# Performance work log

Hardware: AMD Instinct MI355X
Metric: run time of the kernel (lower is better)

Reference implementation:

```python
import jax, jax.numpy as jnp
import numpy as np

N = 262144            # inflated nodes (atoms + edge-nodes)
E = 4 * 1024 * 1024   # directed edges
D = 8                 # node_feature_dim
TD = 1                # time_dim
H = 32                # hidden_channels
L = 4                 # num_layers
BN_EPS = 1e-5


def setup_inputs() -> dict:
    key = jax.random.key(0)
    ks = jax.random.split(key, 12)
    s = 0.1  # small init scale
    return {
        "x": jax.random.normal(ks[0], (N, D), jnp.float32),
        "t": jax.random.uniform(ks[1], (1,), jnp.float32),
        "edge_index": jax.random.randint(ks[2], (2, E), 0, N, jnp.int32),
        "node_mask": jax.random.randint(ks[3], (N,), 0, 2) > 0,
        "edge_mask": jax.random.randint(ks[4], (N,), 0, 2) > 0,
        "ond": 5,  # original_node_feature_dim
        "oed": 4,  # original_edge_feature_dim
        # GINConv MLP params: layer 0 has in=D+TD, layers 1..3 have in=H
        "W1_first": jax.random.normal(ks[5], (D + TD, H), jnp.float32) * s,
        "b1_first": jnp.zeros((H,), jnp.float32),
        "W2_first": jax.random.normal(ks[6], (H, H), jnp.float32) * s,
        "b2_first": jnp.zeros((H,), jnp.float32),
        "W1_rest": jax.random.normal(ks[7], (L - 1, H, H), jnp.float32) * s,
        "b1_rest": jnp.zeros((L - 1, H), jnp.float32),
        "W2_rest": jax.random.normal(ks[8], (L - 1, H, H), jnp.float32) * s,
        "b2_rest": jnp.zeros((L - 1, H), jnp.float32),
        "eps": jnp.zeros((L,), jnp.float32),           # train_eps=True, init 0
        "bn_gamma": jnp.ones((L, H), jnp.float32),
        "bn_beta": jnp.zeros((L, H), jnp.float32),
        "lin_W": jax.random.normal(ks[9], (L * H, D), jnp.float32) * s,
        "lin_b": jnp.zeros((D,), jnp.float32),
    }


def _gin_forward(x, t, W1_first, b1_first, W2_first, b2_first,
                 W1_rest, b1_rest, W2_rest, b2_rest, eps, bn_gamma, bn_beta,
                 lin_W, lin_b, edge_index, node_mask, edge_mask, ond, oed):
    src = edge_index[0]
    dst = edge_index[1]
    n = x.shape[0]
    # x_in = cat(x, t*ones)
    tcol = jnp.full((n, 1), t[0], x.dtype)
    h = jnp.concatenate([x, tcol], axis=1)  # [N, D+TD]
    xs = []
    for l in range(L):
        # GINConv: (1+eps)*x_i + sum_{j->i} x_j, then 2-layer MLP
        agg = jax.ops.segment_sum(h[src], dst, num_segments=n)  # scatter-add
        z = (1.0 + eps[l]) * h + agg
        W1 = W1_first if l == 0 else W1_rest[l - 1]
        b1 = b1_first if l == 0 else b1_rest[l - 1]
        W2 = W2_first if l == 0 else W2_rest[l - 1]
        b2 = b2_first if l == 0 else b2_rest[l - 1]
        z = jax.nn.relu(z @ W1 + b1) @ W2 + b2  # [N, H]
        # BatchNorm (training-mode batch stats), then ReLU; dropout=eval->id
        mu = jnp.mean(z, axis=0)
        var = jnp.var(z, axis=0)
        z = (z - mu) * jax.lax.rsqrt(var + BN_EPS) * bn_gamma[l] + bn_beta[l]
        h = jax.nn.relu(z)
        xs.append(h)
    # JK 'cat' + final Linear(L*H -> D)
    new_x = jnp.concatenate(xs, axis=1) @ lin_W + lin_b  # [N, D]
    # masked feature write-back: x[mask, 1:dim+1] = new_x[mask, 1:dim+1]
    cols = jnp.arange(x.shape[1])
    ncols = (cols >= 1) & (cols < ond + 1)
    ecols = (cols >= 1) & (cols < oed + 1)
    out = jnp.where(node_mask[:, None] & ncols[None, :], new_x, x)
    out = jnp.where(edge_mask[:, None] & ecols[None, :], new_x, out)
    return out


def reference(x, t, edge_index, node_mask, edge_mask, ond, oed,
              W1_first, b1_first, W2_first, b2_first,
              W1_rest, b1_rest, W2_rest, b2_rest,
              eps, bn_gamma, bn_beta, lin_W, lin_b):
    return _gin_forward(x, t, W1_first, b1_first, W2_first, b2_first,
                        W1_rest, b1_rest, W2_rest, b2_rest,
                        eps, bn_gamma, bn_beta, lin_W, lin_b,
                        edge_index, node_mask, edge_mask, ond, oed)
```

## Files before the change

kernel.cpp:

```cpp
#include <hip/hip_runtime.h>
#include <cstdint>

#define NN 262144
#define EE 4194304
#define CAP 64
#define NB 512
#define BSZ 512
#define NSH 8
#define SCAP 1280
#define EPB 4096
#define SLICES 64

typedef __attribute__((ext_vector_type(8))) short bf16x8;
typedef __attribute__((ext_vector_type(4))) float f32x4;
typedef __attribute__((ext_vector_type(2))) float f32x2;
#define MFMA16 __builtin_amdgcn_mfma_f32_16x16x32_bf16

__device__ inline float bf2f(unsigned short u) {
  union { unsigned int i; float f; } v; v.i = ((unsigned int)u) << 16; return v.f;
}
__device__ inline unsigned short f2bf(float f) {
  union { float f; unsigned int i; } v; v.f = f;
  unsigned int r = v.i + 0x7FFF + ((v.i >> 16) & 1);
  return (unsigned short)(r >> 16);
}
__device__ inline float blo(unsigned int u) {
  union { unsigned int i; float f; } v; v.i = u << 16; return v.f;
}
__device__ inline float bhi(unsigned int u) {
  union { unsigned int i; float f; } v; v.i = u & 0xFFFF0000u; return v.f;
}
__device__ inline f32x2 bfpair(unsigned int u) {
  union { unsigned int i; float f; } lo, hi;
  lo.i = u << 16; hi.i = u & 0xFFFF0000u;
  return (f32x2){lo.f, hi.f};
}

__global__ void k_prep(int* __restrict__ cur,
                       const float* __restrict__ W1f, const float* __restrict__ W2f,
                       const float* __restrict__ W1r, const float* __restrict__ W2r,
                       unsigned short* __restrict__ wimg) {
  int tid = threadIdx.x;
  if (blockIdx.x < 16) {
    int i = blockIdx.x * 256 + tid;
    if (i < NSH * NB) cur[i] = i * SCAP;
    return;
  }
  for (int k = tid; k < 4 * 4 * 1280; k += 256) wimg[k] = 0;
  __syncthreads();
  for (int l = 0; l < 4; ++l) {
    const float* W1 = (l == 0) ? W1f : W1r + (size_t)(l - 1) * 1024;
    const float* W2 = (l == 0) ? W2f : W2r + (size_t)(l - 1) * 1024;
    int kdim = (l == 0) ? 9 : 32;
    unsigned short* bm = wimg + (size_t)l * 5120;
    for (int e = tid; e < kdim * 32; e += 256) {
      int k = e >> 5, n = e & 31;
      float v = W1[e];
      unsigned short h = f2bf(v);
      int idx = n * 40 + (k ^ (n & 8));
      bm[idx] = h;
      bm[1280 + idx] = f2bf(v - bf2f(h));
    }
    for (int e = tid; e < 1024; e += 256) {
      int k = e >> 5, n = e & 31;
      float v = W2[e];
      unsigned short h = f2bf(v);
      int idx = n * 40 + (k ^ (n & 8));
      bm[2560 + idx] = h;
      bm[3840 + idx] = f2bf(v - bf2f(h));
    }
  }
}

__global__ void __launch_bounds__(256, 1)
k_bin(const int* __restrict__ ei, int* __restrict__ cur, int* __restrict__ pair) {
  __shared__ int hist[NB];
  __shared__ int off[NB];
  __shared__ int gbase[NB];
  __shared__ int psum[256];
  __shared__ int ebuf[EPB];
  const int tid = threadIdx.x, blk = blockIdx.x, sh = blk & (NSH - 1);
  const int* esrc = ei + (size_t)blk * EPB;
  const int* edst = ei + EE + (size_t)blk * EPB;

  for (int k = tid; k < NB; k += 256) hist[k] = 0;
  __syncthreads();
  for (int j = tid; j < EPB / 4; j += 256) {
    int4 d4 = ((const int4*)edst)[j];
    atomicAdd(&hist[d4.x >> 9], 1);
    atomicAdd(&hist[d4.y >> 9], 1);
    atomicAdd(&hist[d4.z >> 9], 1);
    atomicAdd(&hist[d4.w >> 9], 1);
  }
  __syncthreads();
  int a0 = hist[2 * tid], a1 = hist[2 * tid + 1];
  int ps = a0 + a1;
  psum[tid] = ps;
  __syncthreads();
  for (int d = 1; d < 256; d <<= 1) {
    int v = (tid >= d) ? psum[tid - d] : 0;
    __syncthreads();
    psum[tid] += v;
    __syncthreads();
  }
  int excl = psum[tid] - ps;
  off[2 * tid] = excl;
  off[2 * tid + 1] = excl + a0;
  __syncthreads();
  for (int b = tid; b < NB; b += 256) {
    int n = hist[b];
    int ci = sh * NB + b;
    gbase[b] = n ? atomicAdd(&cur[ci], n) : ci * SCAP;
  }
  __syncthreads();
  for (int k = tid; k < NB; k += 256) hist[k] = off[k];
  __syncthreads();
  for (int j = tid; j < EPB / 4; j += 256) {
    int4 s4 = ((const int4*)esrc)[j];
    int4 d4 = ((const int4*)edst)[j];
    int dd[4] = {d4.x, d4.y, d4.z, d4.w};
    int ss[4] = {s4.x, s4.y, s4.z, s4.w};
#pragma unroll
    for (int u = 0; u < 4; ++u) {
      int bin = dd[u] >> 9, dl = dd[u] & (BSZ - 1);
      int p = atomicAdd(&hist[bin], 1);
      ebuf[p] = ss[u] | (dl << 18);
    }
  }
  __syncthreads();
  for (int b = tid; b < NB; b += 256) {
    int st = off[b];
    int n = hist[b] - st;
    int ci = sh * NB + b;
    int gb = gbase[b];
    int lim = ci * SCAP + SCAP;
    if (gb + n > lim) n = (lim > gb) ? (lim - gb) : 0;
    for (int k = 0; k < n; ++k) pair[gb + k] = ebuf[st + k];
  }
}

__global__ void k_expand(const int* __restrict__ cur, const int* __restrict__ pair,
                         int* __restrict__ slot, int* __restrict__ deg) {
  __shared__ int cbin[BSZ];
  int tid = threadIdx.x;
  int bin = blockIdx.x;
  for (int k = tid; k < BSZ; k += 512) cbin[k] = 0;
  __syncthreads();
  for (int s = 0; s < NSH; ++s) {
    int ci = s * NB + bin, base = ci * SCAP;
    int cnt = min(cur[ci] - base, SCAP);
    for (int k = tid; k < cnt; k += 512) {
      int p = pair[base + k];
      int src = p & 0x3FFFF, dl = p >> 18;
      int pos = atomicAdd(&cbin[dl], 1);
      if (pos < CAP)
        slot[((size_t)bin * BSZ + dl) * CAP + pos] = src;
    }
  }
  __syncthreads();
  for (int k = tid; k < BSZ; k += 512) {
    int cnt = min(cbin[k], CAP);
    int cntp = (cnt + 7) & ~7;
    int self = bin * BSZ + k;
    for (int p = cnt; p < cntp; ++p)
      slot[((size_t)bin * BSZ + k) * CAP + p] = self;
    deg[bin * BSZ + k] = cnt;
  }
}

__global__ void k_layer0(const float* __restrict__ x, const float* __restrict__ t,
                         const int* __restrict__ slot, const int* __restrict__ deg,
                         const unsigned short* __restrict__ wimg,
                         const float* __restrict__ b1, const float* __restrict__ b2,
                         const float* __restrict__ epsv,
                         unsigned short* __restrict__ zb,
                         float* __restrict__ ssum, float* __restrict__ ssq) {
  __shared__ __align__(16) unsigned short insh[640], insl[640], z1h[640], z1l[640];
  __shared__ float aggs0[2][8][8];
  int tid = threadIdx.x;
  int c = tid & 31, g = tid >> 5;
  int w = tid >> 6, lane = tid & 63;
  int m = lane & 15, gk = lane >> 4;
  int nsel = (w & 1) * 16 + m;
  int kbp = (gk * 8) ^ (m & 8);
  int aoff = m * 40 + kbp;
  int boff = nsel * 40 + kbp;
  size_t base = (size_t)blockIdx.x * 16;

  bf16x8 w1hf, w1lf, w2hf, w2lf;
  float bias1 = 0.f, bias2 = 0.f;
  if (w < 2) {
    w1hf = *(const bf16x8*)&wimg[boff];
    w1lf = *(const bf16x8*)&wimg[1280 + boff];
    w2hf = *(const bf16x8*)&wimg[2560 + boff];
    w2lf = *(const bf16x8*)&wimg[3840 + boff];
    bias1 = b1[nsel];
    bias2 = b2[nsel];
  }
  for (int k = tid; k < 640; k += 256) { insh[k] = 0; insl[k] = 0; }

  float t0 = t[0];
  float epsl = epsv[0];
  size_t i0 = base + g, i1 = base + g + 8;
  int cnt0 = deg[i0], cnt1 = deg[i1];
  int cntp0 = (cnt0 + 7) & ~7, cntp1 = (cnt1 + 7) & ~7;
  const int* sl0 = slot + i0 * CAP;
  const int* sl1 = slot + i1 * CAP;
  int sv0 = sl0[c], sv1 = sl1[c];
  float xs0 = (c < 8) ? x[i0 * 8 + c] : 0.f;
  float xs1 = (c < 8) ? x[i1 * 8 + c] : 0.f;

  int q = c & 3, sub = c >> 2;
  const float2* x2 = (const float2*)x;
  f32x2 ac0 = {0.f, 0.f}, ac1 = {0.f, 0.f};
  int km0 = min(cntp0, 32), km1 = min(cntp1, 32);
  int kb_ = min(km0, km1);
  for (int k = 0; k < kb_; k += 8) {
    int s0 = __shfl(sv0, k + sub, 32);
    int s1 = __shfl(sv1, k + sub, 32);
    float2 v0 = x2[(size_t)s0 * 4 + q];
    float2 v1 = x2[(size_t)s1 * 4 + q];
    ac0 += (f32x2){v0.x, v0.y};
    ac1 += (f32x2){v1.x, v1.y};
  }
  for (int k = kb_; k < km0; k += 8) {
    int s0 = __shfl(sv0, k + sub, 32);
    float2 v0 = x2[(size_t)s0 * 4 + q];
    ac0 += (f32x2){v0.x, v0.y};
  }
  for (int k = kb_; k < km1; k += 8) {
    int s1 = __shfl(sv1, k + sub, 32);
    float2 v1 = x2[(size_t)s1 * 4 + q];
    ac1 += (f32x2){v1.x, v1.y};
  }
  if (cntp0 > 32) {
    int sv2 = sl0[32 + c];
    for (int k = 32; k < cntp0; k += 8) {
      int s0 = __shfl(sv2, k - 32 + sub, 32);
      float2 v0 = x2[(size_t)s0 * 4 + q];
      ac0 += (f32x2){v0.x, v0.y};
    }
  }
  if (cntp1 > 32) {
    int sv2 = sl1[32 + c];
    for (int k = 32; k < cntp1; k += 8) {
      int s1 = __shfl(sv2, k - 32 + sub, 32);
      float2 v1 = x2[(size_t)s1 * 4 + q];
      ac1 += (f32x2){v1.x, v1.y};
    }
  }
#pragma unroll
  for (int off = 4; off < 32; off <<= 1) {
    ac0.x += __shfl_xor(ac0.x, off, 32);
    ac0.y += __shfl_xor(ac0.y, off, 32);
    ac1.x += __shfl_xor(ac1.x, off, 32);
    ac1.y += __shfl_xor(ac1.y, off, 32);
  }
  if (c < 4) {
    aggs0[0][g][2 * c] = ac0.x; aggs0[0][g][2 * c + 1] = ac0.y;
    aggs0[1][g][2 * c] = ac1.x; aggs0[1][g][2 * c + 1] = ac1.y;
  }
  __syncthreads();
  if (c < 9) {
    float p0 = (float)(cntp0 - cnt0), p1 = (float)(cntp1 - cnt1);
    float inv0 = (c < 8) ? ((1.f + epsl) * xs0 + aggs0[0][g][c] - p0 * xs0)
                         : ((1.f + epsl) * t0 + (float)cnt0 * t0);
    float inv1 = (c < 8) ? ((1.f + epsl) * xs1 + aggs0[1][g][c] - p1 * xs1)
                         : ((1.f + epsl) * t0 + (float)cnt1 * t0);
    int ii0 = g * 40 + c;
    int ii1 = (g + 8) * 40 + (c ^ 8);
    unsigned short h0 = f2bf(inv0), h1 = f2bf(inv1);
    insh[ii0] = h0; insl[ii0] = f2bf(inv0 - bf2f(h0));
    insh[ii1] = h1; insl[ii1] = f2bf(inv1 - bf2f(h1));
  }
  __syncthreads();

  if (w < 2) {
    bf16x8 ah = *(const bf16x8*)&insh[aoff];
    bf16x8 al = *(const bf16x8*)&insl[aoff];
    f32x4 c1 = {0.f, 0.f, 0.f, 0.f};
    c1 = MFMA16(ah, w1hf, c1, 0, 0, 0);
    c1 = MFMA16(al, w1hf, c1, 0, 0, 0);
    c1 = MFMA16(ah, w1lf, c1, 0, 0, 0);
#pragma unroll
    for (int r = 0; r < 4; ++r) {
      int rr = gk * 4 + r;
      float z = fmaxf(c1[r] + bias1, 0.f);
      unsigned short h = f2bf(z);
      int zi = rr * 40 + (nsel ^ (rr & 8));
      z1h[zi] = h;
      z1l[zi] = f2bf(z - bf2f(h));
    }
  }
  __syncthreads();
  if (w < 2) {
    bf16x8 ah = *(const bf16x8*)&z1h[aoff];
    bf16x8 al = *(const bf16x8*)&z1l[aoff];
    f32x4 c2 = {0.f, 0.f, 0.f, 0.f};
    c2 = MFMA16(ah, w2hf, c2, 0, 0, 0);
    c2 = MFMA16(al, w2hf, c2, 0, 0, 0);
    c2 = MFMA16(ah, w2lf, c2, 0, 0, 0);
    float s1 = 0.f, s2 = 0.f;
#pragma unroll
    for (int r = 0; r < 4; ++r) {
      int rr = gk * 4 + r;
      float z = c2[r] + bias2;
      zb[(base + rr) * 32 + nsel] = f2bf(z);
      s1 += z; s2 += z * z;
    }
    s1 += __shfl_xor(s1, 16, 64); s2 += __shfl_xor(s2, 16, 64);
    s1 += __shfl_xor(s1, 32, 64); s2 += __shfl_xor(s2, 32, 64);
    if (gk == 0) {
      int slice = blockIdx.x & (SLICES - 1);
      atomicAdd(&ssum[slice * 32 + nsel], s1);
      atomicAdd(&ssq[slice * 32 + nsel], s2);
    }
  }
}

__global__ void k_bnapply(const unsigned short* __restrict__ zb,
                          const float* __restrict__ ssum, const float* __restrict__ ssq,
                          const float* __restrict__ gamma, const float* __restrict__ beta,
                          const float* __restrict__ linW,
                          unsigned short* __restrict__ hb,
                          float* __restrict__ out_acc, int first_acc) {
  __shared__ float linWs[256];
  __shared__ float scs[32], shs[32];
  int tid = threadIdx.x;
  for (int k = tid; k < 256; k += 256) linWs[k] = linW[k];
  if (tid < 32) {
    float s1 = 0.f, s2 = 0.f;
    for (int s = 0; s < SLICES; ++s) { s1 += ssum[s * 32 + tid]; s2 += ssq[s * 32 + tid]; }
    float mu = s1 * (1.f / NN);
    float var = s2 * (1.f / NN) - mu * mu;
    float sc = gamma[tid] * rsqrtf(var + 1e-5f);
    scs[tid] = sc;
    shs[tid] = beta[tid] - mu * sc;
  }
  int r = tid & 3;
  size_t n = (size_t)blockIdx.x * 64 + (tid >> 2);
  uint4 u = ((const uint4*)zb)[n * 4 + r];
  __syncthreads();

  float h[8];
#pragma unroll
  for (int j = 0; j < 8; ++j) {
    unsigned int w = (j < 2) ? u.x : (j < 4) ? u.y : (j < 6) ? u.z : u.w;
    float zv = (j & 1) ? bhi(w) : blo(w);
    h[j] = fmaxf(zv * scs[8 * r + j] + shs[8 * r + j], 0.f);
  }
  uint4 o;
  o.x = (unsigned int)f2bf(h[0]) | ((unsigned int)f2bf(h[1]) << 16);
  o.y = (unsigned int)f2bf(h[2]) | ((unsigned int)f2bf(h[3]) << 16);
  o.z = (unsigned int)f2bf(h[4]) | ((unsigned int)f2bf(h[5]) << 16);
  o.w = (unsigned int)f2bf(h[6]) | ((unsigned int)f2bf(h[7]) << 16);
  ((uint4*)hb)[n * 4 + r] = o;

  float jk[8];
#pragma unroll
  for (int d = 0; d < 8; ++d) {
    float a = 0.f;
#pragma unroll
    for (int j = 0; j < 8; ++j) a += h[j] * linWs[(8 * r + j) * 8 + d];
    jk[d] = a;
  }
#pragma unroll
  for (int off = 1; off <= 2; off <<= 1)
#pragma unroll
    for (int d = 0; d < 8; ++d) jk[d] += __shfl_xor(jk[d], off, 64);
  if (r == 0) {
    float4 a0 = {jk[0], jk[1], jk[2], jk[3]};
    float4 a1 = {jk[4], jk[5], jk[6], jk[7]};
    if (!first_acc) {
      float4 p0 = ((const float4*)out_acc)[n * 2];
      float4 p1 = ((const float4*)out_acc)[n * 2 + 1];
      a0.x += p0.x; a0.y += p0.y; a0.z += p0.z; a0.w += p0.w;
      a1.x += p1.x; a1.y += p1.y; a1.z += p1.z; a1.w += p1.w;
    }
    ((float4*)out_acc)[n * 2] = a0;
    ((float4*)out_acc)[n * 2 + 1] = a1;
  }
}

__global__ void k_layerN(const unsigned short* __restrict__ hb,
                         const int* __restrict__ slot, const int* __restrict__ deg,
                         const unsigned short* __restrict__ wimg,
                         const float* __restrict__ b1, const float* __restrict__ b2,
                         const float* __restrict__ epsv, int l,
                         unsigned short* __restrict__ zbo,
                         float* __restrict__ ssum, float* __restrict__ ssq) {
  __shared__ __align__(16) unsigned short insh[640], insl[640], z1h[640], z1l[640];
  __shared__ float aggs[2][8][32];
  int tid = threadIdx.x;
  int c = tid & 31, g = tid >> 5;
  int w = tid >> 6, lane = tid & 63;
  int m = lane & 15, gk = lane >> 4;
  int nsel = (w & 1) * 16 + m;
  int kbp = (gk * 8) ^ (m & 8);
  int aoff = m * 40 + kbp;
  int boff = nsel * 40 + kbp;
  size_t base = (size_t)blockIdx.x * 16;

  const unsigned short* wl = wimg + (size_t)l * 5120;
  bf16x8 w1hf, w1lf, w2hf, w2lf;
  float bias1 = 0.f, bias2 = 0.f;
  if (w < 2) {
    w1hf = *(const bf16x8*)&wl[boff];
    w1lf = *(const bf16x8*)&wl[1280 + boff];
    w2hf = *(const bf16x8*)&wl[2560 + boff];
    w2lf = *(const bf16x8*)&wl[3840 + boff];
    bias1 = b1[nsel];
    bias2 = b2[nsel];
  }

  float epsl = epsv[l];
  size_t i0 = base + g, i1 = base + g + 8;
  int cnt0 = deg[i0], cnt1 = deg[i1];
  int cntp0 = (cnt0 + 7) & ~7, cntp1 = (cnt1 + 7) & ~7;
  const int* sl0 = slot + i0 * CAP;
  const int* sl1 = slot + i1 * CAP;
  int sv0 = sl0[c], sv1 = sl1[c];
  float hs0 = bf2f(hb[i0 * 32 + c]);
  float hs1 = bf2f(hb[i1 * 32 + c]);

  int q = c & 7, sub = c >> 3;
  const uint2* h2 = (const uint2*)hb;
  f32x2 a001 = {0.f, 0.f}, a023 = {0.f, 0.f};
  f32x2 a101 = {0.f, 0.f}, a123 = {0.f, 0.f};
  int km0 = min(cntp0, 32), km1 = min(cntp1, 32);
  int kb_ = min(km0, km1);
  for (int k = 0; k < kb_; k += 8) {
    int sa0 = __shfl(sv0, k + sub, 32);
    int sb0 = __shfl(sv0, k + 4 + sub, 32);
    int sa1 = __shfl(sv1, k + sub, 32);
    int sb1 = __shfl(sv1, k + 4 + sub, 32);
    uint2 ua = h2[(size_t)sa0 * 8 + q];
    uint2 ub = h2[(size_t)sb0 * 8 + q];
    uint2 uc = h2[(size_t)sa1 * 8 + q];
    uint2 ud = h2[(size_t)sb1 * 8 + q];
    a001 += bfpair(ua.x); a023 += bfpair(ua.y);
    a001 += bfpair(ub.x); a023 += bfpair(ub.y);
    a101 += bfpair(uc.x); a123 += bfpair(uc.y);
    a101 += bfpair(ud.x); a123 += bfpair(ud.y);
  }
  for (int k = kb_; k < km0; k += 8) {
    int sa0 = __shfl(sv0, k + sub, 32);
    int sb0 = __shfl(sv0, k + 4 + sub, 32);
    uint2 ua = h2[(size_t)sa0 * 8 + q];
    uint2 ub = h2[(size_t)sb0 * 8 + q];
    a001 += bfpair(ua.x); a023 += bfpair(ua.y);
    a001 += bfpair(ub.x); a023 += bfpair(ub.y);
  }
  for (int k = kb_; k < km1; k += 8) {
    int sa1 = __shfl(sv1, k + sub, 32);
    int sb1 = __shfl(sv1, k + 4 + sub, 32);
    uint2 uc = h2[(size_t)sa1 * 8 + q];
    uint2 ud = h2[(size_t)sb1 * 8 + q];
    a101 += bfpair(uc.x); a123 += bfpair(uc.y);
    a101 += bfpair(ud.x); a123 += bfpair(ud.y);
  }
  if (cntp0 > 32) {
    int sv2 = sl0[32 + c];
    for (int k = 32; k < cntp0; k += 8) {
      int sa0 = __shfl(sv2, k - 32 + sub, 32);
      int sb0 = __shfl(sv2, k - 28 + sub, 32);
      uint2 ua = h2[(size_t)sa0 * 8 + q];
      uint2 ub = h2[(size_t)sb0 * 8 + q];
      a001 += bfpair(ua.x); a023 += bfpair(ua.y);
      a001 += bfpair(ub.x); a023 += bfpair(ub.y);
    }
  }
  if (cntp1 > 32) {
    int sv2 = sl1[32 + c];
    for (int k = 32; k < cntp1; k += 8) {
      int sa1 = __shfl(sv2, k - 32 + sub, 32);
      int sb1 = __shfl(sv2, k - 28 + sub, 32);
      uint2 uc = h2[(size_t)sa1 * 8 + q];
      uint2 ud = h2[(size_t)sb1 * 8 + q];
      a101 += bfpair(uc.x); a123 += bfpair(uc.y);
      a101 += bfpair(ud.x); a123 += bfpair(ud.y);
    }
  }
  a001.x += __shfl_xor(a001.x, 8, 32); a001.x += __shfl_xor(a001.x, 16, 32);
  a001.y += __shfl_xor(a001.y, 8, 32); a001.y += __shfl_xor(a001.y, 16, 32);
  a023.x += __shfl_xor(a023.x, 8, 32); a023.x += __shfl_xor(a023.x, 16, 32);
  a023.y += __shfl_xor(a023.y, 8, 32); a023.y += __shfl_xor(a023.y, 16, 32);
  a101.x += __shfl_xor(a101.x, 8, 32); a101.x += __shfl_xor(a101.x, 16, 32);
  a101.y += __shfl_xor(a101.y, 8, 32); a101.y += __shfl_xor(a101.y, 16, 32);
  a123.x += __shfl_xor(a123.x, 8, 32); a123.x += __shfl_xor(a123.x, 16, 32);
  a123.y += __shfl_xor(a123.y, 8, 32); a123.y += __shfl_xor(a123.y, 16, 32);
  if (c < 8) {
    *(float4*)&aggs[0][g][q * 4] = make_float4(a001.x, a001.y, a023.x, a023.y);
    *(float4*)&aggs[1][g][q * 4] = make_float4(a101.x, a101.y, a123.x, a123.y);
  }
  __syncthreads();
  {
    float s0 = aggs[0][g][c];
    float s1 = aggs[1][g][c];
    float inv0 = (1.f + epsl - (float)(cntp0 - cnt0)) * hs0 + s0;
    float inv1 = (1.f + epsl - (float)(cntp1 - cnt1)) * hs1 + s1;
    int ii0 = g * 40 + c;
    int ii1 = (g + 8) * 40 + (c ^ 8);
    unsigned short h0 = f2bf(inv0), h1 = f2bf(inv1);
    insh[ii0] = h0; insl[ii0] = f2bf(inv0 - bf2f(h0));
    insh[ii1] = h1; insl[ii1] = f2bf(inv1 - bf2f(h1));
  }
  __syncthreads();

  if (w < 2) {
    bf16x8 ah = *(const bf16x8*)&insh[aoff];
    bf16x8 al = *(const bf16x8*)&insl[aoff];
    f32x4 c1 = {0.f, 0.f, 0.f, 0.f};
    c1 = MFMA16(ah, w1hf, c1, 0, 0, 0);
    c1 = MFMA16(al, w1hf, c1, 0, 0, 0);
    c1 = MFMA16(ah, w1lf, c1, 0, 0, 0);
#pragma unroll
    for (int r = 0; r < 4; ++r) {
      int rr = gk * 4 + r;
      float z = fmaxf(c1[r] + bias1, 0.f);
      unsigned short h = f2bf(z);
      int zi = rr * 40 + (nsel ^ (rr & 8));
      z1h[zi] = h;
      z1l[zi] = f2bf(z - bf2f(h));
    }
  }
  __syncthreads();
  if (w < 2) {
    bf16x8 ah = *(const bf16x8*)&z1h[aoff];
    bf16x8 al = *(const bf16x8*)&z1l[aoff];
    f32x4 c2 = {0.f, 0.f, 0.f, 0.f};
    c2 = MFMA16(ah, w2hf, c2, 0, 0, 0);
    c2 = MFMA16(al, w2hf, c2, 0, 0, 0);
    c2 = MFMA16(ah, w2lf, c2, 0, 0, 0);
    float s1 = 0.f, s2 = 0.f;
#pragma unroll
    for (int r = 0; r < 4; ++r) {
      int rr = gk * 4 + r;
      float z = c2[r] + bias2;
      zbo[(base + rr) * 32 + nsel] = f2bf(z);
      s1 += z; s2 += z * z;
    }
    s1 += __shfl_xor(s1, 16, 64); s2 += __shfl_xor(s2, 16, 64);
    s1 += __shfl_xor(s1, 32, 64); s2 += __shfl_xor(s2, 32, 64);
    if (gk == 0) {
      int slice = blockIdx.x & (SLICES - 1);
      atomicAdd(&ssum[slice * 32 + nsel], s1);
      atomicAdd(&ssq[slice * 32 + nsel], s2);
    }
  }
}

__global__ void k_final(const unsigned short* __restrict__ z3,
                        const float* __restrict__ ssum, const float* __restrict__ ssq,
                        const float* __restrict__ gamma, const float* __restrict__ beta,
                        const float* __restrict__ linW3, const float* __restrict__ lin_b,
                        const float* __restrict__ out_acc, const float* __restrict__ x,
                        const int* __restrict__ nm, const int* __restrict__ em,
                        const int* __restrict__ ondp, const int* __restrict__ oedp,
                        float* __restrict__ out) {
  __shared__ float linWs[256];
  __shared__ float scs[32], shs[32];
  int tid = threadIdx.x;
  for (int k = tid; k < 256; k += 256) linWs[k] = linW3[k];
  if (tid < 32) {
    float s1 = 0.f, s2 = 0.f;
    for (int s = 0; s < SLICES; ++s) { s1 += ssum[s * 32 + tid]; s2 += ssq[s * 32 + tid]; }
    float mu = s1 * (1.f / NN);
    float var = s2 * (1.f / NN) - mu * mu;
    float sc = gamma[tid] * rsqrtf(var + 1e-5f);
    scs[tid] = sc;
    shs[tid] = beta[tid] - mu * sc;
  }
  int r = tid & 3;
  size_t n = (size_t)blockIdx.x * 64 + (tid >> 2);
  uint4 u = ((const uint4*)z3)[n * 4 + r];
  __syncthreads();

  float h[8];
#pragma unroll
  for (int j = 0; j < 8; ++j) {
    unsigned int w = (j < 2) ? u.x : (j < 4) ? u.y : (j < 6) ? u.z : u.w;
    float zv = (j & 1) ? bhi(w) : blo(w);
    h[j] = fmaxf(zv * scs[8 * r + j] + shs[8 * r + j], 0.f);
  }
  float jk[8];
#pragma unroll
  for (int d = 0; d < 8; ++d) {
    float a = 0.f;
#pragma unroll
    for (int j = 0; j < 8; ++j) a += h[j] * linWs[(8 * r + j) * 8 + d];
    jk[d] = a;
  }
#pragma unroll
  for (int off = 1; off <= 2; off <<= 1)
#pragma unroll
    for (int d = 0; d < 8; ++d) jk[d] += __shfl_xor(jk[d], off, 64);
  if (r == 0) {
    float4 p0 = ((const float4*)out_acc)[n * 2];
    float4 p1 = ((const float4*)out_acc)[n * 2 + 1];
    float4 x0 = ((const float4*)x)[n * 2];
    float4 x1 = ((const float4*)x)[n * 2 + 1];
    float res[8] = {jk[0] + p0.x + lin_b[0], jk[1] + p0.y + lin_b[1],
                    jk[2] + p0.z + lin_b[2], jk[3] + p0.w + lin_b[3],
                    jk[4] + p1.x + lin_b[4], jk[5] + p1.y + lin_b[5],
                    jk[6] + p1.z + lin_b[6], jk[7] + p1.w + lin_b[7]};
    float xs[8] = {x0.x, x0.y, x0.z, x0.w, x1.x, x1.y, x1.z, x1.w};
    int ond = ondp[0], oed = oedp[0];
    bool nmv = nm[n] != 0, emv = em[n] != 0;
    float o[8];
#pragma unroll
    for (int d = 0; d < 8; ++d) {
      bool w = (d >= 1) && ((nmv && d < ond + 1) || (emv && d < oed + 1));
      o[d] = w ? res[d] : xs[d];
    }
    ((float4*)out)[n * 2]     = make_float4(o[0], o[1], o[2], o[3]);
    ((float4*)out)[n * 2 + 1] = make_float4(o[4], o[5], o[6], o[7]);
  }
}

extern "C" void kernel_launch(void* const* d_in, const int* in_sizes, int n_in,
                              void* d_out, int out_size, void* d_ws, size_t ws_size,
                              hipStream_t stream) {
  const float* x        = (const float*)d_in[0];
  const float* t        = (const float*)d_in[1];
  const int*   ei       = (const int*)d_in[2];
  const int*   node_mask= (const int*)d_in[3];
  const int*   edge_mask= (const int*)d_in[4];
  const int*   ondp     = (const int*)d_in[5];
  const int*   oedp     = (const int*)d_in[6];
  const float* W1_first = (const float*)d_in[7];
  const float* b1_first = (const float*)d_in[8];
  const float* W2_first = (const float*)d_in[9];
  const float* b2_first = (const float*)d_in[10];
  const float* W1_rest  = (const float*)d_in[11];
  const float* b1_rest  = (const float*)d_in[12];
  const float* W2_rest  = (const float*)d_in[13];
  const float* b2_rest  = (const float*)d_in[14];
  const float* epsv     = (const float*)d_in[15];
  const float* bn_gamma = (const float*)d_in[16];
  const float* bn_beta  = (const float*)d_in[17];
  const float* lin_W    = (const float*)d_in[18];
  const float* lin_b    = (const float*)d_in[19];
  float* out = (float*)d_out;

  char* ws = (char*)d_ws;
  size_t off = 0;
  int*   slot    = (int*)(ws + off);   off += (size_t)NN * CAP * 4;
  int*   pair    = (int*)(ws + off);   off += (size_t)NSH * NB * SCAP * 4;
  int*   cur     = (int*)(ws + off);   off += (size_t)NSH * NB * 4;
  int*   deg     = (int*)(ws + off);   off += (size_t)NN * 4;
  unsigned short* zb = (unsigned short*)(ws + off); off += (size_t)NN * 32 * 2;
  unsigned short* hb = (unsigned short*)(ws + off); off += (size_t)NN * 32 * 2;
  float* out_acc = (float*)(ws + off); off += (size_t)NN * 8 * 4;
  float* stats   = (float*)(ws + off); off += (size_t)4 * 2 * SLICES * 32 * 4;
  unsigned short* wimg = (unsigned short*)(ws + off); off += (size_t)4 * 4 * 1280 * 2;
  (void)ws_size; (void)in_sizes; (void)n_in; (void)out_size;

  hipMemsetAsync(stats, 0, (size_t)4 * 2 * SLICES * 32 * 4, stream);
  k_prep<<<17, 256, 0, stream>>>(cur, W1_first, W2_first, W1_rest, W2_rest, wimg);
  k_bin<<<EE / EPB, 256, 0, stream>>>(ei, cur, pair);
  k_expand<<<NB, 512, 0, stream>>>(cur, pair, slot, deg);

  {
    float* ssum = stats;
    float* ssq  = ssum + SLICES * 32;
    k_layer0<<<NN / 16, 256, 0, stream>>>(x, t, slot, deg, wimg, b1_first,
                                          b2_first, epsv, zb, ssum, ssq);
    k_bnapply<<<NN / 64, 256, 0, stream>>>(zb, ssum, ssq, bn_gamma, bn_beta,
                                           lin_W, hb, out_acc, 1);
  }
  for (int l = 1; l < 4; ++l) {
    const float* b1 = b1_rest + (size_t)(l - 1) * 32;
    const float* b2 = b2_rest + (size_t)(l - 1) * 32;
    float* ssum = stats + (size_t)l * 2 * SLICES * 32;
    float* ssq  = ssum + SLICES * 32;
    k_layerN<<<NN / 16, 256, 0, stream>>>(hb, slot, deg, wimg, b1, b2,
                                          epsv, l, zb, ssum, ssq);
    if (l < 3)
      k_bnapply<<<NN / 64, 256, 0, stream>>>(zb, ssum, ssq, bn_gamma + l * 32,
                                             bn_beta + l * 32,
                                             lin_W + (size_t)l * 32 * 8,
                                             hb, out_acc, 0);
  }
  k_final<<<NN / 64, 256, 0, stream>>>(zb, stats + 3 * 2 * SLICES * 32,
                                       stats + 3 * 2 * SLICES * 32 + SLICES * 32,
                                       bn_gamma + 96, bn_beta + 96,
                                       lin_W + 3 * 32 * 8, lin_b, out_acc, x,
                                       node_mask, edge_mask, ondp, oedp, out);
}
```

Measured before the change: 517.5 us.

## Sort neighbor slots by source range and loop layer blocks over node sets

k_expand now runs two passes: it counts each destination's edges per 65536-node source quarter, then places them at prefix offsets so every neighbor list is grouped by source range. This is meant to improve cache locality of the gathers. The layer kernels now give each block 8 sets of 16 nodes in a loop, reusing the weight fragments loaded into registers and launching 8x fewer blocks, with launch_bounds(256,4). The costs are an extra pass over pair in k_expand and less parallelism, since barrier stalls now repeat serially within each block.

```diff
diff --git a/kernel.cpp b/kernel.cpp
--- a/kernel.cpp
+++ b/kernel.cpp
@@ -10,6 +10,8 @@
 #define SCAP 1280
 #define EPB 4096
 #define SLICES 64
+#define SETS 8
+#define LGRID (NN / (16 * SETS))
 
 typedef __attribute__((ext_vector_type(8))) short bf16x8;
 typedef __attribute__((ext_vector_type(4))) float f32x4;
@@ -141,10 +143,11 @@
 
 __global__ void k_expand(const int* __restrict__ cur, const int* __restrict__ pair,
                          int* __restrict__ slot, int* __restrict__ deg) {
-  __shared__ int cbin[BSZ];
+  __shared__ int cnt4[BSZ][4];
+  __shared__ int ofs[BSZ][4];
   int tid = threadIdx.x;
   int bin = blockIdx.x;
-  for (int k = tid; k < BSZ; k += 512) cbin[k] = 0;
+  for (int k = tid; k < BSZ * 4; k += 512) ((int*)cnt4)[k] = 0;
   __syncthreads();
   for (int s = 0; s < NSH; ++s) {
     int ci = s * NB + bin, base = ci * SCAP;
@@ -152,14 +155,37 @@
     for (int k = tid; k < cnt; k += 512) {
       int p = pair[base + k];
       int src = p & 0x3FFFF, dl = p >> 18;
-      int pos = atomicAdd(&cbin[dl], 1);
-      if (pos < CAP)
+      atomicAdd(&cnt4[dl][src >> 16], 1);
+    }
+  }
+  __syncthreads();
+  for (int k = tid; k < BSZ; k += 512) {
+    int cum = 0;
+#pragma unroll
+    for (int r = 0; r < 4; ++r) {
+      int c = cnt4[k][r];
+      int s0 = cum;
+      int e = min(cum + c, CAP);
+      ofs[k][r] = s0;
+      cnt4[k][r] = e;
+      cum = e;
+    }
+  }
+  __syncthreads();
+  for (int s = 0; s < NSH; ++s) {
+    int ci = s * NB + bin, base = ci * SCAP;
+    int cnt = min(cur[ci] - base, SCAP);
+    for (int k = tid; k < cnt; k += 512) {
+      int p = pair[base + k];
+      int src = p & 0x3FFFF, dl = p >> 18, r = src >> 16;
+      int pos = atomicAdd(&ofs[dl][r], 1);
+      if (pos < cnt4[dl][r])
         slot[((size_t)bin * BSZ + dl) * CAP + pos] = src;
     }
   }
   __syncthreads();
   for (int k = tid; k < BSZ; k += 512) {
-    int cnt = min(cbin[k], CAP);
+    int cnt = cnt4[k][3];
     int cntp = (cnt + 7) & ~7;
     int self = bin * BSZ + k;
     for (int p = cnt; p < cntp; ++p)
@@ -168,13 +194,14 @@
   }
 }
 
-__global__ void k_layer0(const float* __restrict__ x, const float* __restrict__ t,
-                         const int* __restrict__ slot, const int* __restrict__ deg,
-                         const unsigned short* __restrict__ wimg,
-                         const float* __restrict__ b1, const float* __restrict__ b2,
-                         const float* __restrict__ epsv,
-                         unsigned short* __restrict__ zb,
-                         float* __restrict__ ssum, float* __restrict__ ssq) {
+__global__ void __launch_bounds__(256, 4)
+k_layer0(const float* __restrict__ x, const float* __restrict__ t,
+         const int* __restrict__ slot, const int* __restrict__ deg,
+         const unsigned short* __restrict__ wimg,
+         const float* __restrict__ b1, const float* __restrict__ b2,
+         const float* __restrict__ epsv,
+         unsigned short* __restrict__ zb,
+         float* __restrict__ ssum, float* __restrict__ ssq) {
   __shared__ __align__(16) unsigned short insh[640], insl[640], z1h[640], z1l[640];
   __shared__ float aggs0[2][8][8];
   int tid = threadIdx.x;
@@ -185,7 +212,6 @@
   int kbp = (gk * 8) ^ (m & 8);
   int aoff = m * 40 + kbp;
   int boff = nsel * 40 + kbp;
-  size_t base = (size_t)blockIdx.x * 16;
 
   bf16x8 w1hf, w1lf, w2hf, w2lf;
   float bias1 = 0.f, bias2 = 0.f;
@@ -201,119 +227,123 @@
 
   float t0 = t[0];
   float epsl = epsv[0];
-  size_t i0 = base + g, i1 = base + g + 8;
-  int cnt0 = deg[i0], cnt1 = deg[i1];
-  int cntp0 = (cnt0 + 7) & ~7, cntp1 = (cnt1 + 7) & ~7;
-  const int* sl0 = slot + i0 * CAP;
-  const int* sl1 = slot + i1 * CAP;
-  int sv0 = sl0[c], sv1 = sl1[c];
-  float xs0 = (c < 8) ? x[i0 * 8 + c] : 0.f;
-  float xs1 = (c < 8) ? x[i1 * 8 + c] : 0.f;
-
-  int q = c & 3, sub = c >> 2;
-  const float2* x2 = (const float2*)x;
-  f32x2 ac0 = {0.f, 0.f}, ac1 = {0.f, 0.f};
-  int km0 = min(cntp0, 32), km1 = min(cntp1, 32);
-  int kb_ = min(km0, km1);
-  for (int k = 0; k < kb_; k += 8) {
-    int s0 = __shfl(sv0, k + sub, 32);
-    int s1 = __shfl(sv1, k + sub, 32);
-    float2 v0 = x2[(size_t)s0 * 4 + q];
-    float2 v1 = x2[(size_t)s1 * 4 + q];
-    ac0 += (f32x2){v0.x, v0.y};
-    ac1 += (f32x2){v1.x, v1.y};
-  }
-  for (int k = kb_; k < km0; k += 8) {
-    int s0 = __shfl(sv0, k + sub, 32);
-    float2 v0 = x2[(size_t)s0 * 4 + q];
-    ac0 += (f32x2){v0.x, v0.y};
-  }
-  for (int k = kb_; k < km1; k += 8) {
-    int s1 = __shfl(sv1, k + sub, 32);
-    float2 v1 = x2[(size_t)s1 * 4 + q];
-    ac1 += (f32x2){v1.x, v1.y};
-  }
-  if (cntp0 > 32) {
-    int sv2 = sl0[32 + c];
-    for (int k = 32; k < cntp0; k += 8) {
-      int s0 = __shfl(sv2, k - 32 + sub, 32);
+
+  for (int set = 0; set < SETS; ++set) {
+    size_t base = ((size_t)blockIdx.x * SETS + set) * 16;
+    size_t i0 = base + g, i1 = base + g + 8;
+    int cnt0 = deg[i0], cnt1 = deg[i1];
+    int cntp0 = (cnt0 + 7) & ~7, cntp1 = (cnt1 + 7) & ~7;
+    const int* sl0 = slot + i0 * CAP;
+    const int* sl1 = slot + i1 * CAP;
+    int sv0 = sl0[c], sv1 = sl1[c];
+    float xs0 = (c < 8) ? x[i0 * 8 + c] : 0.f;
+    float xs1 = (c < 8) ? x[i1 * 8 + c] : 0.f;
+
+    int q = c & 3, sub = c >> 2;
+    const float2* x2 = (const float2*)x;
+    f32x2 ac0 = {0.f, 0.f}, ac1 = {0.f, 0.f};
+    int km0 = min(cntp0, 32), km1 = min(cntp1, 32);
+    int kb_ = min(km0, km1);
+    for (int k = 0; k < kb_; k += 8) {
+      int s0 = __shfl(sv0, k + sub, 32);
+      int s1 = __shfl(sv1, k + sub, 32);
+      float2 v0 = x2[(size_t)s0 * 4 + q];
+      float2 v1 = x2[(size_t)s1 * 4 + q];
+      ac0 += (f32x2){v0.x, v0.y};
+      ac1 += (f32x2){v1.x, v1.y};
+    }
+    for (int k = kb_; k < km0; k += 8) {
+      int s0 = __shfl(sv0, k + sub, 32);
       float2 v0 = x2[(size_t)s0 * 4 + q];
       ac0 += (f32x2){v0.x, v0.y};
     }
-  }
-  if (cntp1 > 32) {
-    int sv2 = sl1[32 + c];
-    for (int k = 32; k < cntp1; k += 8) {
-      int s1 = __shfl(sv2, k - 32 + sub, 32);
+    for (int k = kb_; k < km1; k += 8) {
+      int s1 = __shfl(sv1, k + sub, 32);
       float2 v1 = x2[(size_t)s1 * 4 + q];
       ac1 += (f32x2){v1.x, v1.y};
     }
-  }
-#pragma unroll
-  for (int off = 4; off < 32; off <<= 1) {
-    ac0.x += __shfl_xor(ac0.x, off, 32);
-    ac0.y += __shfl_xor(ac0.y, off, 32);
-    ac1.x += __shfl_xor(ac1.x, off, 32);
-    ac1.y += __shfl_xor(ac1.y, off, 32);
-  }
-  if (c < 4) {
-    aggs0[0][g][2 * c] = ac0.x; aggs0[0][g][2 * c + 1] = ac0.y;
-    aggs0[1][g][2 * c] = ac1.x; aggs0[1][g][2 * c + 1] = ac1.y;
-  }
-  __syncthreads();
-  if (c < 9) {
-    float p0 = (float)(cntp0 - cnt0), p1 = (float)(cntp1 - cnt1);
-    float inv0 = (c < 8) ? ((1.f + epsl) * xs0 + aggs0[0][g][c] - p0 * xs0)
-                         : ((1.f + epsl) * t0 + (float)cnt0 * t0);
-    float inv1 = (c < 8) ? ((1.f + epsl) * xs1 + aggs0[1][g][c] - p1 * xs1)
-                         : ((1.f + epsl) * t0 + (float)cnt1 * t0);
-    int ii0 = g * 40 + c;
-    int ii1 = (g + 8) * 40 + (c ^ 8);
-    unsigned short h0 = f2bf(inv0), h1 = f2bf(inv1);
-    insh[ii0] = h0; insl[ii0] = f2bf(inv0 - bf2f(h0));
-    insh[ii1] = h1; insl[ii1] = f2bf(inv1 - bf2f(h1));
-  }
-  __syncthreads();
-
-  if (w < 2) {
-    bf16x8 ah = *(const bf16x8*)&insh[aoff];
-    bf16x8 al = *(const bf16x8*)&insl[aoff];
-    f32x4 c1 = {0.f, 0.f, 0.f, 0.f};
-    c1 = MFMA16(ah, w1hf, c1, 0, 0, 0);
-    c1 = MFMA16(al, w1hf, c1, 0, 0, 0);
-    c1 = MFMA16(ah, w1lf, c1, 0, 0, 0);
-#pragma unroll
-    for (int r = 0; r < 4; ++r) {
-      int rr = gk * 4 + r;
-      float z = fmaxf(c1[r] + bias1, 0.f);
-      unsigned short h = f2bf(z);
-      int zi = rr * 40 + (nsel ^ (rr & 8));
-      z1h[zi] = h;
-      z1l[zi] = f2bf(z - bf2f(h));
-    }
-  }
-  __syncthreads();
-  if (w < 2) {
-    bf16x8 ah = *(const bf16x8*)&z1h[aoff];
-    bf16x8 al = *(const bf16x8*)&z1l[aoff];
-    f32x4 c2 = {0.f, 0.f, 0.f, 0.f};
-    c2 = MFMA16(ah, w2hf, c2, 0, 0, 0);
-    c2 = MFMA16(al, w2hf, c2, 0, 0, 0);
-    c2 = MFMA16(ah, w2lf, c2, 0, 0, 0);
-    float s1 = 0.f, s2 = 0.f;
-#pragma unroll
-    for (int r = 0; r < 4; ++r) {
-      int rr = gk * 4 + r;
-      float z = c2[r] + bias2;
-      zb[(base + rr) * 32 + nsel] = f2bf(z);
-      s1 += z; s2 += z * z;
-    }
-    s1 += __shfl_xor(s1, 16, 64); s2 += __shfl_xor(s2, 16, 64);
-    s1 += __shfl_xor(s1, 32, 64); s2 += __shfl_xor(s2, 32, 64);
-    if (gk == 0) {
-      int slice = blockIdx.x & (SLICES - 1);
-      atomicAdd(&ssum[slice * 32 + nsel], s1);
-      atomicAdd(&ssq[slice * 32 + nsel], s2);
+    if (cntp0 > 32) {
+      int sv2 = sl0[32 + c];
+      for (int k = 32; k < cntp0; k += 8) {
+        int s0 = __shfl(sv2, k - 32 + sub, 32);
+        float2 v0 = x2[(size_t)s0 * 4 + q];
+        ac0 += (f32x2){v0.x, v0.y};
+      }
+    }
+    if (cntp1 > 32) {
+      int sv2 = sl1[32 + c];
+      for (int k = 32; k < cntp1; k += 8) {
+        int s1 = __shfl(sv2, k - 32 + sub, 32);
+        float2 v1 = x2[(size_t)s1 * 4 + q];
+        ac1 += (f32x2){v1.x, v1.y};
+      }
+    }
+#pragma unroll
+    for (int off = 4; off < 32; off <<= 1) {
+      ac0.x += __shfl_xor(ac0.x, off, 32);
+      ac0.y += __shfl_xor(ac0.y, off, 32);
+      ac1.x += __shfl_xor(ac1.x, off, 32);
+      ac1.y += __shfl_xor(ac1.y, off, 32);
+    }
+    if (c < 4) {
+      aggs0[0][g][2 * c] = ac0.x; aggs0[0][g][2 * c + 1] = ac0.y;
+      aggs0[1][g][2 * c] = ac1.x; aggs0[1][g][2 * c + 1] = ac1.y;
+    }
+    __syncthreads();
+    if (c < 9) {
+      float p0 = (float)(cntp0 - cnt0), p1 = (float)(cntp1 - cnt1);
+      float inv0 = (c < 8) ? ((1.f + epsl) * xs0 + aggs0[0][g][c] - p0 * xs0)
+                           : ((1.f + epsl) * t0 + (float)cnt0 * t0);
+      float inv1 = (c < 8) ? ((1.f + epsl) * xs1 + aggs0[1][g][c] - p1 * xs1)
+                           : ((1.f + epsl) * t0 + (float)cnt1 * t0);
+      int ii0 = g * 40 + c;
+      int ii1 = (g + 8) * 40 + (c ^ 8);
+      unsigned short h0 = f2bf(inv0), h1 = f2bf(inv1);
+      insh[ii0] = h0; insl[ii0] = f2bf(inv0 - bf2f(h0));
+      insh[ii1] = h1; insl[ii1] = f2bf(inv1 - bf2f(h1));
+    }
+    __syncthreads();
+
+    if (w < 2) {
+      bf16x8 ah = *(const bf16x8*)&insh[aoff];
+      bf16x8 al = *(const bf16x8*)&insl[aoff];
+      f32x4 c1 = {0.f, 0.f, 0.f, 0.f};
+      c1 = MFMA16(ah, w1hf, c1, 0, 0, 0);
+      c1 = MFMA16(al, w1hf, c1, 0, 0, 0);
+      c1 = MFMA16(ah, w1lf, c1, 0, 0, 0);
+#pragma unroll
+      for (int r = 0; r < 4; ++r) {
+        int rr = gk * 4 + r;
+        float z = fmaxf(c1[r] + bias1, 0.f);
+        unsigned short h = f2bf(z);
+        int zi = rr * 40 + (nsel ^ (rr & 8));
+        z1h[zi] = h;
+        z1l[zi] = f2bf(z - bf2f(h));
+      }
+    }
+    __syncthreads();
+    if (w < 2) {
+      bf16x8 ah = *(const bf16x8*)&z1h[aoff];
+      bf16x8 al = *(const bf16x8*)&z1l[aoff];
+      f32x4 c2 = {0.f, 0.f, 0.f, 0.f};
+      c2 = MFMA16(ah, w2hf, c2, 0, 0, 0);
+      c2 = MFMA16(al, w2hf, c2, 0, 0, 0);
+      c2 = MFMA16(ah, w2lf, c2, 0, 0, 0);
+      float s1 = 0.f, s2 = 0.f;
+#pragma unroll
+      for (int r = 0; r < 4; ++r) {
+        int rr = gk * 4 + r;
+        float z = c2[r] + bias2;
+        zb[(base + rr) * 32 + nsel] = f2bf(z);
+        s1 += z; s2 += z * z;
+      }
+      s1 += __shfl_xor(s1, 16, 64); s2 += __shfl_xor(s2, 16, 64);
+      s1 += __shfl_xor(s1, 32, 64); s2 += __shfl_xor(s2, 32, 64);
+      if (gk == 0) {
+        int slice = blockIdx.x & (SLICES - 1);
+        atomicAdd(&ssum[slice * 32 + nsel], s1);
+        atomicAdd(&ssq[slice * 32 + nsel], s2);
+      }
     }
   }
 }
@@ -382,13 +412,14 @@
   }
 }
 
-__global__ void k_layerN(const unsigned short* __restrict__ hb,
-                         const int* __restrict__ slot, const int* __restrict__ deg,
-                         const unsigned short* __restrict__ wimg,
-                         const float* __restrict__ b1, const float* __restrict__ b2,
-                         const float* __restrict__ epsv, int l,
-                         unsigned short* __restrict__ zbo,
-                         float* __restrict__ ssum, float* __restrict__ ssq) {
+__global__ void __launch_bounds__(256, 4)
+k_layerN(const unsigned short* __restrict__ hb,
+         const int* __restrict__ slot, const int* __restrict__ deg,
+         const unsigned short* __restrict__ wimg,
+         const float* __restrict__ b1, const float* __restrict__ b2,
+         const float* __restrict__ epsv, int l,
+         unsigned short* __restrict__ zbo,
+         float* __restrict__ ssum, float* __restrict__ ssq) {
   __shared__ __align__(16) unsigned short insh[640], insl[640], z1h[640], z1l[640];
   __shared__ float aggs[2][8][32];
   int tid = threadIdx.x;
@@ -399,7 +430,6 @@
   int kbp = (gk * 8) ^ (m & 8);
   int aoff = m * 40 + kbp;
   int boff = nsel * 40 + kbp;
-  size_t base = (size_t)blockIdx.x * 16;
 
   const unsigned short* wl = wimg + (size_t)l * 5120;
   bf16x8 w1hf, w1lf, w2hf, w2lf;
@@ -414,138 +444,142 @@
   }
 
   float epsl = epsv[l];
-  size_t i0 = base + g, i1 = base + g + 8;
-  int cnt0 = deg[i0], cnt1 = deg[i1];
-  int cntp0 = (cnt0 + 7) & ~7, cntp1 = (cnt1 + 7) & ~7;
-  const int* sl0 = slot + i0 * CAP;
-  const int* sl1 = slot + i1 * CAP;
-  int sv0 = sl0[c], sv1 = sl1[c];
-  float hs0 = bf2f(hb[i0 * 32 + c]);
-  float hs1 = bf2f(hb[i1 * 32 + c]);
-
-  int q = c & 7, sub = c >> 3;
-  const uint2* h2 = (const uint2*)hb;
-  f32x2 a001 = {0.f, 0.f}, a023 = {0.f, 0.f};
-  f32x2 a101 = {0.f, 0.f}, a123 = {0.f, 0.f};
-  int km0 = min(cntp0, 32), km1 = min(cntp1, 32);
-  int kb_ = min(km0, km1);
-  for (int k = 0; k < kb_; k += 8) {
-    int sa0 = __shfl(sv0, k + sub, 32);
-    int sb0 = __shfl(sv0, k + 4 + sub, 32);
-    int sa1 = __shfl(sv1, k + sub, 32);
-    int sb1 = __shfl(sv1, k + 4 + sub, 32);
-    uint2 ua = h2[(size_t)sa0 * 8 + q];
-    uint2 ub = h2[(size_t)sb0 * 8 + q];
-    uint2 uc = h2[(size_t)sa1 * 8 + q];
-    uint2 ud = h2[(size_t)sb1 * 8 + q];
-    a001 += bfpair(ua.x); a023 += bfpair(ua.y);
-    a001 += bfpair(ub.x); a023 += bfpair(ub.y);
-    a101 += bfpair(uc.x); a123 += bfpair(uc.y);
-    a101 += bfpair(ud.x); a123 += bfpair(ud.y);
-  }
-  for (int k = kb_; k < km0; k += 8) {
-    int sa0 = __shfl(sv0, k + sub, 32);
-    int sb0 = __shfl(sv0, k + 4 + sub, 32);
-    uint2 ua = h2[(size_t)sa0 * 8 + q];
-    uint2 ub = h2[(size_t)sb0 * 8 + q];
-    a001 += bfpair(ua.x); a023 += bfpair(ua.y);
-    a001 += bfpair(ub.x); a023 += bfpair(ub.y);
-  }
-  for (int k = kb_; k < km1; k += 8) {
-    int sa1 = __shfl(sv1, k + sub, 32);
-    int sb1 = __shfl(sv1, k + 4 + sub, 32);
-    uint2 uc = h2[(size_t)sa1 * 8 + q];
-    uint2 ud = h2[(size_t)sb1 * 8 + q];
-    a101 += bfpair(uc.x); a123 += bfpair(uc.y);
-    a101 += bfpair(ud.x); a123 += bfpair(ud.y);
-  }
-  if (cntp0 > 32) {
-    int sv2 = sl0[32 + c];
-    for (int k = 32; k < cntp0; k += 8) {
-      int sa0 = __shfl(sv2, k - 32 + sub, 32);
-      int sb0 = __shfl(sv2, k - 28 + sub, 32);
+
+  for (int set = 0; set < SETS; ++set) {
+    size_t base = ((size_t)blockIdx.x * SETS + set) * 16;
+    size_t i0 = base + g, i1 = base + g + 8;
+    int cnt0 = deg[i0], cnt1 = deg[i1];
+    int cntp0 = (cnt0 + 7) & ~7, cntp1 = (cnt1 + 7) & ~7;
+    const int* sl0 = slot + i0 * CAP;
+    const int* sl1 = slot + i1 * CAP;
+    int sv0 = sl0[c], sv1 = sl1[c];
+    float hs0 = bf2f(hb[i0 * 32 + c]);
+    float hs1 = bf2f(hb[i1 * 32 + c]);
+
+    int q = c & 7, sub = c >> 3;
+    const uint2* h2 = (const uint2*)hb;
+    f32x2 a001 = {0.f, 0.f}, a023 = {0.f, 0.f};
+    f32x2 a101 = {0.f, 0.f}, a123 = {0.f, 0.f};
+    int km0 = min(cntp0, 32), km1 = min(cntp1, 32);
+    int kb_ = min(km0, km1);
+    for (int k = 0; k < kb_; k += 8) {
+      int sa0 = __shfl(sv0, k + sub, 32);
+      int sb0 = __shfl(sv0, k + 4 + sub, 32);
+      int sa1 = __shfl(sv1, k + sub, 32);
+      int sb1 = __shfl(sv1, k + 4 + sub, 32);
+      uint2 ua = h2[(size_t)sa0 * 8 + q];
+      uint2 ub = h2[(size_t)sb0 * 8 + q];
+      uint2 uc = h2[(size_t)sa1 * 8 + q];
+      uint2 ud = h2[(size_t)sb1 * 8 + q];
+      a001 += bfpair(ua.x); a023 += bfpair(ua.y);
+      a001 += bfpair(ub.x); a023 += bfpair(ub.y);
+      a101 += bfpair(uc.x); a123 += bfpair(uc.y);
+      a101 += bfpair(ud.x); a123 += bfpair(ud.y);
+    }
+    for (int k = kb_; k < km0; k += 8) {
+      int sa0 = __shfl(sv0, k + sub, 32);
+      int sb0 = __shfl(sv0, k + 4 + sub, 32);
       uint2 ua = h2[(size_t)sa0 * 8 + q];
       uint2 ub = h2[(size_t)sb0 * 8 + q];
       a001 += bfpair(ua.x); a023 += bfpair(ua.y);
       a001 += bfpair(ub.x); a023 += bfpair(ub.y);
     }
-  }
-  if (cntp1 > 32) {
-    int sv2 = sl1[32 + c];
-    for (int k = 32; k < cntp1; k += 8) {
-      int sa1 = __shfl(sv2, k - 32 + sub, 32);
-      int sb1 = __shfl(sv2, k - 28 + sub, 32);
+    for (int k = kb_; k < km1; k += 8) {
+      int sa1 = __shfl(sv1, k + sub, 32);
+      int sb1 = __shfl(sv1, k + 4 + sub, 32);
       uint2 uc = h2[(size_t)sa1 * 8 + q];
       uint2 ud = h2[(size_t)sb1 * 8 + q];
       a101 += bfpair(uc.x); a123 += bfpair(uc.y);
       a101 += bfpair(ud.x); a123 += bfpair(ud.y);
     }
-  }
-  a001.x += __shfl_xor(a001.x, 8, 32); a001.x += __shfl_xor(a001.x, 16, 32);
-  a001.y += __shfl_xor(a001.y, 8, 32); a001.y += __shfl_xor(a001.y, 16, 32);
-  a023.x += __shfl_xor(a023.x, 8, 32); a023.x += __shfl_xor(a023.x, 16, 32);
-  a023.y += __shfl_xor(a023.y, 8, 32); a023.y += __shfl_xor(a023.y, 16, 32);
-  a101.x += __shfl_xor(a101.x, 8, 32); a101.x += __shfl_xor(a101.x, 16, 32);
-  a101.y += __shfl_xor(a101.y, 8, 32); a101.y += __shfl_xor(a101.y, 16, 32);
-  a123.x += __shfl_xor(a123.x, 8, 32); a123.x += __shfl_xor(a123.x, 16, 32);
-  a123.y += __shfl_xor(a123.y, 8, 32); a123.y += __shfl_xor(a123.y, 16, 32);
-  if (c < 8) {
-    *(float4*)&aggs[0][g][q * 4] = make_float4(a001.x, a001.y, a023.x, a023.y);
-    *(float4*)&aggs[1][g][q * 4] = make_float4(a101.x, a101.y, a123.x, a123.y);
-  }
-  __syncthreads();
-  {
-    float s0 = aggs[0][g][c];
-    float s1 = aggs[1][g][c];
-    float inv0 = (1.f + epsl - (float)(cntp0 - cnt0)) * hs0 + s0;
-    float inv1 = (1.f + epsl - (float)(cntp1 - cnt1)) * hs1 + s1;
-    int ii0 = g * 40 + c;
-    int ii1 = (g + 8) * 40 + (c ^ 8);
-    unsigned short h0 = f2bf(inv0), h1 = f2bf(inv1);
-    insh[ii0] = h0; insl[ii0] = f2bf(inv0 - bf2f(h0));
-    insh[ii1] = h1; insl[ii1] = f2bf(inv1 - bf2f(h1));
-  }
-  __syncthreads();
-
-  if (w < 2) {
-    bf16x8 ah = *(const bf16x8*)&insh[aoff];
-    bf16x8 al = *(const bf16x8*)&insl[aoff];
-    f32x4 c1 = {0.f, 0.f, 0.f, 0.f};
-    c1 = MFMA16(ah, w1hf, c1, 0, 0, 0);
-    c1 = MFMA16(al, w1hf, c1, 0, 0, 0);
-    c1 = MFMA16(ah, w1lf, c1, 0, 0, 0);
-#pragma unroll
-    for (int r = 0; r < 4; ++r) {
-      int rr = gk * 4 + r;
-      float z = fmaxf(c1[r] + bias1, 0.f);
-      unsigned short h = f2bf(z);
-      int zi = rr * 40 + (nsel ^ (rr & 8));
-      z1h[zi] = h;
-      z1l[zi] = f2bf(z - bf2f(h));
-    }
-  }
-  __syncthreads();
-  if (w < 2) {
-    bf16x8 ah = *(const bf16x8*)&z1h[aoff];
-    bf16x8 al = *(const bf16x8*)&z1l[aoff];
-    f32x4 c2 = {0.f, 0.f, 0.f, 0.f};
-    c2 = MFMA16(ah, w2hf, c2, 0, 0, 0);
-    c2 = MFMA16(al, w2hf, c2, 0, 0, 0);
-    c2 = MFMA16(ah, w2lf, c2, 0, 0, 0);
-    float s1 = 0.f, s2 = 0.f;
-#pragma unroll
-    for (int r = 0; r < 4; ++r) {
-      int rr = gk * 4 + r;
-      float z = c2[r] + bias2;
-      zbo[(base + rr) * 32 + nsel] = f2bf(z);
-      s1 += z; s2 += z * z;
-    }
-    s1 += __shfl_xor(s1, 16, 64); s2 += __shfl_xor(s2, 16, 64);
-    s1 += __shfl_xor(s1, 32, 64); s2 += __shfl_xor(s2, 32, 64);
-    if (gk == 0) {
-      int slice = blockIdx.x & (SLICES - 1);
-      atomicAdd(&ssum[slice * 32 + nsel], s1);
-      atomicAdd(&ssq[slice * 32 + nsel], s2);
+    if (cntp0 > 32) {
+      int sv2 = sl0[32 + c];
+      for (int k = 32; k < cntp0; k += 8) {
+        int sa0 = __shfl(sv2, k - 32 + sub, 32);
+        int sb0 = __shfl(sv2, k - 28 + sub, 32);
+        uint2 ua = h2[(size_t)sa0 * 8 + q];
+        uint2 ub = h2[(size_t)sb0 * 8 + q];
+        a001 += bfpair(ua.x); a023 += bfpair(ua.y);
+        a001 += bfpair(ub.x); a023 += bfpair(ub.y);
+      }
+    }
+    if (cntp1 > 32) {
+      int sv2 = sl1[32 + c];
+      for (int k = 32; k < cntp1; k += 8) {
+        int sa1 = __shfl(sv2, k - 32 + sub, 32);
+        int sb1 = __shfl(sv2, k - 28 + sub, 32);
+        uint2 uc = h2[(size_t)sa1 * 8 + q];
+        uint2 ud = h2[(size_t)sb1 * 8 + q];
+        a101 += bfpair(uc.x); a123 += bfpair(uc.y);
+        a101 += bfpair(ud.x); a123 += bfpair(ud.y);
+      }
+    }
+    a001.x += __shfl_xor(a001.x, 8, 32); a001.x += __shfl_xor(a001.x, 16, 32);
+    a001.y += __shfl_xor(a001.y, 8, 32); a001.y += __shfl_xor(a001.y, 16, 32);
+    a023.x += __shfl_xor(a023.x, 8, 32); a023.x += __shfl_xor(a023.x, 16, 32);
+    a023.y += __shfl_xor(a023.y, 8, 32); a023.y += __shfl_xor(a023.y, 16, 32);
+    a101.x += __shfl_xor(a101.x, 8, 32); a101.x += __shfl_xor(a101.x, 16, 32);
+    a101.y += __shfl_xor(a101.y, 8, 32); a101.y += __shfl_xor(a101.y, 16, 32);
+    a123.x += __shfl_xor(a123.x, 8, 32); a123.x += __shfl_xor(a123.x, 16, 32);
+    a123.y += __shfl_xor(a123.y, 8, 32); a123.y += __shfl_xor(a123.y, 16, 32);
+    if (c < 8) {
+      *(float4*)&aggs[0][g][q * 4] = make_float4(a001.x, a001.y, a023.x, a023.y);
+      *(float4*)&aggs[1][g][q * 4] = make_float4(a101.x, a101.y, a123.x, a123.y);
+    }
+    __syncthreads();
+    {
+      float s0 = aggs[0][g][c];
+      float s1 = aggs[1][g][c];
+      float inv0 = (1.f + epsl - (float)(cntp0 - cnt0)) * hs0 + s0;
+      float inv1 = (1.f + epsl - (float)(cntp1 - cnt1)) * hs1 + s1;
+      int ii0 = g * 40 + c;
+      int ii1 = (g + 8) * 40 + (c ^ 8);
+      unsigned short h0 = f2bf(inv0), h1 = f2bf(inv1);
+      insh[ii0] = h0; insl[ii0] = f2bf(inv0 - bf2f(h0));
+      insh[ii1] = h1; insl[ii1] = f2bf(inv1 - bf2f(h1));
+    }
+    __syncthreads();
+
+    if (w < 2) {
+      bf16x8 ah = *(const bf16x8*)&insh[aoff];
+      bf16x8 al = *(const bf16x8*)&insl[aoff];
+      f32x4 c1 = {0.f, 0.f, 0.f, 0.f};
+      c1 = MFMA16(ah, w1hf, c1, 0, 0, 0);
+      c1 = MFMA16(al, w1hf, c1, 0, 0, 0);
+      c1 = MFMA16(ah, w1lf, c1, 0, 0, 0);
+#pragma unroll
+      for (int r = 0; r < 4; ++r) {
+        int rr = gk * 4 + r;
+        float z = fmaxf(c1[r] + bias1, 0.f);
+        unsigned short h = f2bf(z);
+        int zi = rr * 40 + (nsel ^ (rr & 8));
+        z1h[zi] = h;
+        z1l[zi] = f2bf(z - bf2f(h));
+      }
+    }
+    __syncthreads();
+    if (w < 2) {
+      bf16x8 ah = *(const bf16x8*)&z1h[aoff];
+      bf16x8 al = *(const bf16x8*)&z1l[aoff];
+      f32x4 c2 = {0.f, 0.f, 0.f, 0.f};
+      c2 = MFMA16(ah, w2hf, c2, 0, 0, 0);
+      c2 = MFMA16(al, w2hf, c2, 0, 0, 0);
+      c2 = MFMA16(ah, w2lf, c2, 0, 0, 0);
+      float s1 = 0.f, s2 = 0.f;
+#pragma unroll
+      for (int r = 0; r < 4; ++r) {
+        int rr = gk * 4 + r;
+        float z = c2[r] + bias2;
+        zbo[(base + rr) * 32 + nsel] = f2bf(z);
+        s1 += z; s2 += z * z;
+      }
+      s1 += __shfl_xor(s1, 16, 64); s2 += __shfl_xor(s2, 16, 64);
+      s1 += __shfl_xor(s1, 32, 64); s2 += __shfl_xor(s2, 32, 64);
+      if (gk == 0) {
+        int slice = blockIdx.x & (SLICES - 1);
+        atomicAdd(&ssum[slice * 32 + nsel], s1);
+        atomicAdd(&ssq[slice * 32 + nsel], s2);
+      }
     }
   }
 }
@@ -664,8 +698,8 @@
   {
     float* ssum = stats;
     float* ssq  = ssum + SLICES * 32;
-    k_layer0<<<NN / 16, 256, 0, stream>>>(x, t, slot, deg, wimg, b1_first,
-                                          b2_first, epsv, zb, ssum, ssq);
+    k_layer0<<<LGRID, 256, 0, stream>>>(x, t, slot, deg, wimg, b1_first,
+                                        b2_first, epsv, zb, ssum, ssq);
     k_bnapply<<<NN / 64, 256, 0, stream>>>(zb, ssum, ssq, bn_gamma, bn_beta,
                                            lin_W, hb, out_acc, 1);
   }
@@ -674,8 +708,8 @@
     const float* b2 = b2_rest + (size_t)(l - 1) * 32;
     float* ssum = stats + (size_t)l * 2 * SLICES * 32;
     float* ssq  = ssum + SLICES * 32;
-    k_layerN<<<NN / 16, 256, 0, stream>>>(hb, slot, deg, wimg, b1, b2,
-                                          epsv, l, zb, ssum, ssq);
+    k_layerN<<<LGRID, 256, 0, stream>>>(hb, slot, deg, wimg, b1, b2,
+                                        epsv, l, zb, ssum, ssq);
     if (l < 3)
       k_bnapply<<<NN / 64, 256, 0, stream>>>(zb, ssum, ssq, bn_gamma + l * 32,
                                              bn_beta + l * 32,
```

Result: slower. 562.2 us (+8.6%).
